# Optimization experiments

Hardware: AMD Instinct MI355X
Metric: run time of the kernel (lower is better)

## Reference

```python
import jax, jax.numpy as jnp
import numpy as np

SR = 24000
N_FFT = 1024
HOP = 320
N_MELS = 128
N_CB = 4
VOCAB = 1024
D_MODEL = 512


def _mel_fbanks():
    # torchaudio melscale_fbanks defaults: htk mel scale, norm=None, f_min=0, f_max=sr/2
    n_freqs = N_FFT // 2 + 1
    all_freqs = np.linspace(0.0, SR / 2.0, n_freqs)
    hz2mel = lambda f: 2595.0 * np.log10(1.0 + f / 700.0)
    m_pts = np.linspace(hz2mel(0.0), hz2mel(SR / 2.0), N_MELS + 2)
    f_pts = 700.0 * (10.0 ** (m_pts / 2595.0) - 1.0)
    f_diff = np.diff(f_pts)
    slopes = f_pts[None, :] - all_freqs[:, None]          # (n_freqs, n_mels+2)
    down = -slopes[:, :-2] / f_diff[:-1]
    up = slopes[:, 2:] / f_diff[1:]
    return np.maximum(0.0, np.minimum(down, up)).astype(np.float32)  # (n_freqs, n_mels)

_FB = jnp.asarray(_mel_fbanks())
# periodic Hann window (torch.hann_window default)
_WIN = jnp.asarray((0.5 * (1.0 - np.cos(2.0 * np.pi * np.arange(N_FFT) / N_FFT))).astype(np.float32))


def _log_mel(wav):
    # wav: (B, L). center=True STFT with reflect padding, power=2 spectrogram.
    pad = N_FFT // 2
    x = jnp.pad(wav, ((0, 0), (pad, pad)), mode='reflect')
    n_frames = 1 + (x.shape[1] - N_FFT) // HOP
    idx = HOP * jnp.arange(n_frames)[:, None] + jnp.arange(N_FFT)[None, :]
    frames = x[:, idx] * _WIN                              # (B, T, n_fft)
    spec = jnp.abs(jnp.fft.rfft(frames, axis=-1)) ** 2     # (B, T, n_freqs)
    mel = spec @ _FB                                       # (B, T, n_mels)
    return jnp.log(jnp.clip(mel, 1e-5))


def _conv1d(x, w, b):
    # x: (B, C, T), w: (O, I, 3), padding=1
    y = jax.lax.conv_general_dilated(x, w, window_strides=(1,), padding=((1, 1),),
                                     dimension_numbers=('NCH', 'OIH', 'NCH'))
    return y + b[None, :, None]


def setup_inputs() -> dict:
    key = jax.random.key(0)
    k = jax.random.split(key, 4)
    waveform = jax.random.normal(k[0], (16, 240000), dtype=jnp.float32)
    w1 = jax.random.normal(k[1], (256, N_MELS, 3), dtype=jnp.float32) * 0.05
    b1 = jnp.zeros((256,), dtype=jnp.float32)
    w2 = jax.random.normal(k[2], (D_MODEL, 256, 3), dtype=jnp.float32) * 0.05
    b2 = jnp.zeros((D_MODEL,), dtype=jnp.float32)
    codebooks = jax.random.normal(k[3], (N_CB, VOCAB, D_MODEL // N_CB), dtype=jnp.float32)
    return {"waveform": waveform, "w1": w1, "b1": b1, "w2": w2, "b2": b2, "codebooks": codebooks}


def reference(waveform, w1, b1, w2, b2, codebooks):
    logmel = _log_mel(waveform)                            # (B, T, n_mels)
    x = logmel.transpose(0, 2, 1)                          # (B, n_mels, T)
    h = jax.nn.gelu(_conv1d(x, w1, b1), approximate=False)
    feats = _conv1d(h, w2, b2).transpose(0, 2, 1)          # (B, T, D_MODEL)
    B, T, D = feats.shape
    f4 = feats.reshape(B, T, N_CB, D // N_CB)              # per-codebook slices
    x2 = jnp.sum(f4 * f4, axis=-1)[..., None]              # (B, T, K, 1)
    c2 = jnp.sum(codebooks * codebooks, axis=-1)           # (K, V)
    xc = jnp.einsum('btkd,kvd->btkv', f4, codebooks)       # (B, T, K, V)
    d2 = x2 - 2.0 * xc + c2[None, None]
    tokens = jnp.argmin(d2, axis=-1)                       # (B, T, K)
    return tokens.transpose(0, 2, 1).astype(jnp.int32)     # (B, n_codebooks, T)
```

## Files before the change

kernel.cpp:

```cpp
#include <hip/hip_runtime.h>
#include <hip/hip_bf16.h>
#include <float.h>

#define PI_D 3.14159265358979323846

#define LWAV 240000
#define TFR  751
#define BATCH 16
#define MROWS (BATCH * TFR)
#define NMEL 128
#define TFRP 753
#define PITCH2 12160
#define MTILES 95
#define MAXW 40

#define BSWZ(c) ((c) ^ ((((c) >> 5) & 3) << 2))

#define OFF_WIN    0u
#define OFF_TW512  4096u
#define OFF_UTW    8192u
#define OFF_C2MX   12304u
#define OFF_CNT    12352u
#define OFF_MELW   16384u
#define OFF_MELSL  36864u
#define OFF_WB1    40960u
#define OFF_WBH2   434176u
#define OFF_WBL2   1220608u
#define OFF_PB     434176u
#define OFF_C2     2007040u
#define OFF_CBH    2023424u
#define OFF_CBL    3072000u
#define OFF_X2     4120576u
#define OFF_HT     4317184u
#define OFF_FET    16777216u
#define OFF_LMT    OFF_FET
#define OFF_LIST   OFF_FET
#define WS_NEEDED  41685000u

typedef unsigned short u16;
typedef __attribute__((ext_vector_type(8))) __bf16 bf16x8;
typedef __attribute__((ext_vector_type(4))) float f32x4;
union UB { uint4 u; bf16x8 v; };
union UA { u16 s[8]; bf16x8 v; };

__device__ __forceinline__ u16 bf16rne(float x) {
  unsigned u = __float_as_uint(x);
  return (u16)((u + 0x7FFFu + ((u >> 16) & 1u)) >> 16);
}
__device__ __forceinline__ float bf16tof(u16 h) {
  return __uint_as_float(((unsigned)h) << 16);
}

__global__ void k_setup_tab(float* __restrict__ win, float2* __restrict__ tw512,
                            float2* __restrict__ utw) {
  int t = threadIdx.x;
  if (t < 1024) {
    double v = 0.5 * (1.0 - cos(2.0 * PI_D * (double)t / 1024.0));
    win[t] = (float)v;
  }
  if (t < 512) {
    double a = -2.0 * PI_D * (double)t / 512.0;
    tw512[t] = make_float2((float)cos(a), (float)sin(a));
  }
  if (t < 513) {
    double a = -2.0 * PI_D * (double)t / 1024.0;
    utw[t] = make_float2((float)cos(a), (float)sin(a));
  }
}

__device__ __forceinline__ double fpt_d(int j) {
  double melmax = 2595.0 * log10(1.0 + 12000.0 / 700.0);
  double mp = melmax * (double)j / 129.0;
  return 700.0 * (pow(10.0, mp / 2595.0) - 1.0);
}

__global__ void k_melw(float* __restrict__ melw, int2* __restrict__ melsl) {
  int m = threadIdx.x;
  double f0 = fpt_d(m), f1 = fpt_d(m + 1), f2 = fpt_d(m + 2);
  const double binw = 12000.0 / 512.0;
  int s = (int)floor(f0 / binw) + 1;
  if (s < 0) s = 0;
  int e = (int)ceil(f2 / binw) - 1;
  if (e > 512) e = 512;
  int len = e - s + 1;
  if (len < 0) len = 0;
  if (len > MAXW) len = MAXW;
  melsl[m] = make_int2(s, len);
  for (int j = 0; j < MAXW; ++j) {
    double freq = binw * (double)(s + j);
    double down = (freq - f0) / (f1 - f0);
    double up = (f2 - freq) / (f2 - f1);
    double v = fmin(down, up);
    v = fmax(0.0, v);
    melw[m * MAXW + j] = (j < len) ? (float)v : 0.f;
  }
}

__global__ void k_wt(const float* __restrict__ w, float* __restrict__ wt,
                     int O, int C) {
  int idx = blockIdx.x * 256 + threadIdx.x;
  int total = O * C * 3;
  if (idx >= total) return;
  int o = idx % O;
  int rest = idx / O;
  int i = rest % C;
  int dt = rest / C;
  wt[(dt * C + i) * O + o] = w[(o * C + i) * 3 + dt];
}

__global__ void k_wt2conv(const float* __restrict__ w2, u16* __restrict__ wbH2,
                          u16* __restrict__ wbL2) {
  int idx = blockIdx.x * 256 + threadIdx.x;
  if (idx >= 512 * 768) return;
  int o = idx / 768;
  int k = idx - o * 768;
  int dt = k >> 8, i = k & 255;
  float x = w2[(size_t)(o * 256 + i) * 3 + dt];
  u16 hh = bf16rne(x);
  wbH2[idx] = hh;
  wbL2[idx] = bf16rne(x - bf16tof(hh));
}

__global__ void k_c2(const float* __restrict__ cb, float* __restrict__ c2) {
  int v = blockIdx.x * 256 + threadIdx.x;
  if (v >= 4096) return;
  const float* r = cb + (size_t)v * 128;
  float s = 0.f;
#pragma unroll 8
  for (int i = 0; i < 128; ++i) s = fmaf(r[i], r[i], s);
  c2[v] = s;
}

__global__ void k_c2mx(const float* __restrict__ c2, float* __restrict__ c2mx,
                       unsigned* __restrict__ cnt) {
  __shared__ float red[256];
  int cb = blockIdx.x, tid = threadIdx.x;
  float m = 0.f;
  for (int v = tid; v < 1024; v += 256) m = fmaxf(m, c2[cb * 1024 + v]);
  red[tid] = m;
  __syncthreads();
  for (int s = 128; s > 0; s >>= 1) {
    if (tid < s) red[tid] = fmaxf(red[tid], red[tid + s]);
    __syncthreads();
  }
  if (tid == 0) {
    c2mx[cb] = red[0];
    if (cb == 0) *cnt = 0u;
  }
}

__global__ void k_cbconv(const float* __restrict__ cbs, u16* __restrict__ cbH,
                         u16* __restrict__ cbL) {
  int id = blockIdx.x * 256 + threadIdx.x;
  int v = id >> 5, d4 = (id & 31) * 4;
  float4 x = *(const float4*)(cbs + (size_t)v * 128 + d4);
  const float xs[4] = {x.x, x.y, x.z, x.w};
  unsigned wh[2], wl[2];
#pragma unroll
  for (int p = 0; p < 2; ++p) {
    u16 h0 = bf16rne(xs[2 * p]);
    u16 h1 = bf16rne(xs[2 * p + 1]);
    u16 l0 = bf16rne(xs[2 * p] - bf16tof(h0));
    u16 l1 = bf16rne(xs[2 * p + 1] - bf16tof(h1));
    wh[p] = (unsigned)h0 | ((unsigned)h1 << 16);
    wl[p] = (unsigned)l0 | ((unsigned)l1 << 16);
  }
  *(uint2*)(cbH + (size_t)v * 128 + d4) = make_uint2(wh[0], wh[1]);
  *(uint2*)(cbL + (size_t)v * 128 + d4) = make_uint2(wl[0], wl[1]);
}

__global__ void k_zerocols(float* __restrict__ a, int rows) {
  int tid = blockIdx.x * 256 + threadIdx.x;
  int col_id = tid & 31;
  int r = tid >> 5;
  if (r >= rows) return;
  int bq = col_id >> 1;
  int c = bq * TFRP + ((col_id & 1) ? 752 : 0);
  a[(size_t)r * PITCH2 + c] = 0.f;
}

__device__ __forceinline__ float2 cadd(float2 a, float2 b) { return make_float2(a.x + b.x, a.y + b.y); }
__device__ __forceinline__ float2 csub(float2 a, float2 b) { return make_float2(a.x - b.x, a.y - b.y); }
__device__ __forceinline__ float2 cmul(float2 a, float2 b) {
  return make_float2(a.x * b.x - a.y * b.y, a.x * b.y + a.y * b.x);
}
__device__ __forceinline__ float2 mulnegi(float2 a) { return make_float2(a.y, -a.x); }

__device__ __forceinline__ void dft8(const float2* d, float2* o) {
  const float S = 0.70710678118654752440f;
  float2 f0 = cadd(d[0], d[4]), f1 = csub(d[0], d[4]);
  float2 f2 = cadd(d[2], d[6]), f3 = csub(d[2], d[6]);
  float2 h0 = cadd(d[1], d[5]), h1 = csub(d[1], d[5]);
  float2 h2 = cadd(d[3], d[7]), h3 = csub(d[3], d[7]);
  float2 E0 = cadd(f0, f2), E2 = csub(f0, f2);
  float2 nif3 = mulnegi(f3);
  float2 E1 = cadd(f1, nif3), E3 = csub(f1, nif3);
  float2 O0 = cadd(h0, h2), O2 = csub(h0, h2);
  float2 nih3 = mulnegi(h3);
  float2 O1 = cadd(h1, nih3), O3 = csub(h1, nih3);
  float2 w1o = make_float2(S * (O1.x + O1.y), S * (O1.y - O1.x));
  float2 w2o = mulnegi(O2);
  float2 w3o = make_float2(S * (O3.y - O3.x), -S * (O3.x + O3.y));
  o[0] = cadd(E0, O0);  o[4] = csub(E0, O0);
  o[1] = cadd(E1, w1o); o[5] = csub(E1, w1o);
  o[2] = cadd(E2, w2o); o[6] = csub(E2, w2o);
  o[3] = cadd(E3, w3o); o[7] = csub(E3, w3o);
}

__device__ __forceinline__ float powspec(const float2* Z, const float2* __restrict__ utw,
                                         int k) {
  float2 Zk = Z[k & 511];
  float2 Zm = Z[(512 - k) & 511];
  float2 ut = utw[k];
  float fer = 0.5f * (Zk.x + Zm.x);
  float fei = 0.5f * (Zk.y - Zm.y);
  float fo_r = 0.5f * (Zk.y + Zm.y);
  float fo_i = -0.5f * (Zk.x - Zm.x);
  float xr = fer + ut.x * fo_r - ut.y * fo_i;
  float xi = fei + ut.x * fo_i + ut.y * fo_r;
  return xr * xr + xi * xi;
}

__global__ __launch_bounds__(256) void k_logmel3(
    const float* __restrict__ wav, const float* __restrict__ win,
    const float2* __restrict__ tw512, const float2* __restrict__ utw,
    const float* __restrict__ melw, const int2* __restrict__ melsl,
    float* __restrict__ lmT) {
  __shared__ float2 zbuf[4][512];
  __shared__ float pbuf[4][516];
  __shared__ float mex[128][5];

  const int w = threadIdx.x >> 6;
  const int t = threadIdx.x & 63;
  const int bq = blockIdx.x / 188;
  const int t0 = (blockIdx.x % 188) * 4;
  const int tt = min(t0 + w, TFR - 1);
  const float* wv = wav + (size_t)bq * LWAV;
  float2* Z = zbuf[w];
  float* p = pbuf[w];

  const int base = tt * 320 - 512;

  float2 c[8];
  if (base >= 0 && base + 1024 <= LWAV) {
    const float2* wv2 = (const float2*)(wv + base);
    const float2* wn2 = (const float2*)win;
#pragma unroll
    for (int j = 0; j < 8; ++j) {
      int mm = t + 64 * j;
      float2 xv = wv2[mm];
      float2 wn = wn2[mm];
      c[j] = make_float2(xv.x * wn.x, xv.y * wn.y);
    }
  } else {
#pragma unroll
    for (int j = 0; j < 8; ++j) {
      int mm = t + 64 * j;
      int n0 = base + 2 * mm, n1 = n0 + 1;
      int j0 = n0 < 0 ? -n0 : (n0 >= LWAV ? 2 * LWAV - 2 - n0 : n0);
      int j1 = n1 < 0 ? -n1 : (n1 >= LWAV ? 2 * LWAV - 2 - n1 : n1);
      c[j] = make_float2(wv[j0] * win[2 * mm], wv[j1] * win[2 * mm + 1]);
    }
  }

  float2 e[8];
  dft8(c, e);
#pragma unroll
  for (int pp = 1; pp < 8; ++pp) e[pp] = cmul(e[pp], tw512[(t * pp) & 511]);
#pragma unroll
  for (int pp = 0; pp < 8; ++pp) Z[pp * 64 + (t ^ (pp << 3))] = e[pp];
  asm volatile("s_waitcnt lgkmcnt(0)" ::: "memory");

  const int P = t >> 3, M = t & 7;
  float2 g[8];
#pragma unroll
  for (int v = 0; v < 8; ++v) g[v] = Z[P * 64 + ((M + 8 * v) ^ (P << 3))];
  asm volatile("s_waitcnt lgkmcnt(0)" ::: "memory");

  float2 y[8];
  dft8(g, y);
#pragma unroll
  for (int aa = 1; aa < 8; ++aa) y[aa] = cmul(y[aa], tw512[(8 * M * aa) & 511]);
#pragma unroll
  for (int aa = 0; aa < 8; ++aa) Z[aa * 64 + (((M << 3) + P) ^ (aa << 3))] = y[aa];
  asm volatile("s_waitcnt lgkmcnt(0)" ::: "memory");

  float2 yv[8];
#pragma unroll
  for (int u = 0; u < 8; ++u) yv[u] = Z[P * 64 + (((u << 3) + M) ^ (P << 3))];
  asm volatile("s_waitcnt lgkmcnt(0)" ::: "memory");

  float2 X[8];
  dft8(yv, X);
#pragma unroll
  for (int bb = 0; bb < 8; ++bb) Z[bb * 64 + t] = X[bb];
  asm volatile("s_waitcnt lgkmcnt(0)" ::: "memory");

#pragma unroll
  for (int j = 0; j < 8; ++j) {
    int k = t + 64 * j;
    p[k] = powspec(Z, utw, k);
  }
  if (t == 0) p[512] = powspec(Z, utw, 512);
  asm volatile("s_waitcnt lgkmcnt(0)" ::: "memory");

#pragma unroll
  for (int h = 0; h < 2; ++h) {
    int m = 2 * t + h;
    int2 sl = melsl[m];
    float acc = 0.f;
    const float* wrow = melw + m * MAXW;
    for (int j = 0; j < sl.y; ++j) acc = fmaf(p[sl.x + j], wrow[j], acc);
    mex[m][w] = logf(fmaxf(acc, 1e-5f));
  }
  __syncthreads();
  if (threadIdx.x < 128) {
    int cc = threadIdx.x;
    float* op = lmT + (size_t)cc * PITCH2 + (size_t)bq * TFRP + 1 + t0;
    op[0] = mex[cc][0];
    op[1] = mex[cc][1];
    op[2] = mex[cc][2];
    op[3] = mex[cc][3];
  }
}

template <int C, int N, int BN, bool GELU>
__global__ __launch_bounds__(256) void k_conv64(const float* __restrict__ in,
                                                const float* __restrict__ wt,
                                                const float* __restrict__ bias,
                                                float* __restrict__ out) {
  constexpr int K = 3 * C;
  constexpr int NC = BN / 16;
  __shared__ float At[32 * 64];
  __shared__ float Bt[32 * BN];
  const int m0 = blockIdx.x * 64;
  const int n0 = blockIdx.y * BN;
  const int tid = threadIdx.x;
  const int tm = tid >> 4, tn = tid & 15;

  int bco[NC / 4];
#pragma unroll
  for (int i = 0; i < NC / 4; ++i) bco[i] = BSWZ(tn * NC + i * 4);

  float acc[4][NC] = {};

  for (int k0 = 0; k0 < K; k0 += 32) {
    const int dt = k0 / C;
    const int i0 = k0 - dt * C;
    const float* asrc = in + (size_t)i0 * PITCH2 + (m0 + dt - 1);
    const float* bsrc = wt + (size_t)k0 * N + n0;
#pragma unroll
    for (int h = 0; h < 2; ++h) {
      const int id = tid + h * 256;
      const int r = id >> 4, cf = (id & 15) * 4;
      const float* ap = asrc + (size_t)r * PITCH2 + cf;
      *(float4*)&At[r * 64 + cf] = make_float4(ap[0], ap[1], ap[2], ap[3]);
    }
#pragma unroll
    for (int h = 0; h < BN / 32; ++h) {
      const int id = tid + h * 256;
      const int r = id / (BN / 4), cf = (id % (BN / 4)) * 4;
      *(float4*)&Bt[r * BN + BSWZ(cf)] = *(const float4*)(bsrc + (size_t)r * N + cf);
    }
    __syncthreads();
#pragma unroll
    for (int kc = 0; kc < 32; ++kc) {
      float4 a = *(const float4*)&At[kc * 64 + tm * 4];
      float av[4] = {a.x, a.y, a.z, a.w};
      float bv[NC];
#pragma unroll
      for (int i = 0; i < NC / 4; ++i) {
        float4 b = *(const float4*)&Bt[kc * BN + bco[i]];
        bv[i * 4] = b.x; bv[i * 4 + 1] = b.y; bv[i * 4 + 2] = b.z; bv[i * 4 + 3] = b.w;
      }
#pragma unroll
      for (int r = 0; r < 4; ++r)
#pragma unroll
        for (int cq = 0; cq < NC; ++cq) acc[r][cq] = fmaf(av[r], bv[cq], acc[r][cq]);
    }
    __syncthreads();
  }

#pragma unroll
  for (int cq = 0; cq < NC; ++cq) {
    const int n = n0 + tn * NC + cq;
    const float bb = bias[n];
    float vv[4];
#pragma unroll
    for (int r = 0; r < 4; ++r) {
      float v = acc[r][cq] + bb;
      if (GELU) v = 0.5f * v * (1.0f + erff(v * 0.7071067811865476f));
      vv[r] = v;
    }
    *(float4*)(out + (size_t)n * PITCH2 + m0 + tm * 4) =
        make_float4(vv[0], vv[1], vv[2], vv[3]);
  }
}

#define MFMA16(a, b, c) __builtin_amdgcn_mfma_f32_16x16x32_bf16((a), (b), (c), 0, 0, 0)

#define C2M_ISSUE_A(dst, cc) do {                                           \
    const int kc0_ = (cc) * 32;                                             \
    const int dt_ = kc0_ >> 8, i0_ = kc0_ & 255;                            \
    const float* hb_ = hT + (size_t)(i0_ + g * 8) * PITCH2                  \
                       + m0 + mhalf * 32 + ln + dt_ - 1;                    \
    _Pragma("unroll") for (int mi_ = 0; mi_ < 2; ++mi_)                     \
      _Pragma("unroll") for (int j_ = 0; j_ < 8; ++j_)                      \
        dst[mi_][j_] = hb_[(size_t)j_ * PITCH2 + mi_ * 16];                 \
  } while (0)

#define C2M_ISSUE_B(cc) do {                                                \
    const int kc0_ = (cc) * 32;                                             \
    _Pragma("unroll") for (int h2_ = 0; h2_ < 2; ++h2_) {                   \
      const int id_ = tid + h2_ * 256;                                      \
      const int nn_ = id_ >> 2, part_ = id_ & 3;                            \
      const size_t src_ = (size_t)(n0 + nn_) * 768 + kc0_ + part_ * 8;      \
      rBh[h2_] = *(const uint4*)(wbH2 + src_);                              \
      rBl[h2_] = *(const uint4*)(wbL2 + src_);                              \
    }                                                                       \
  } while (0)

#define C2M_COMMIT_B(buf) do {                                              \
    _Pragma("unroll") for (int h2_ = 0; h2_ < 2; ++h2_) {                   \
      const int id_ = tid + h2_ * 256;                                      \
      const int nn_ = id_ >> 2, part_ = id_ & 3;                            \
      *(uint4*)&bHs[buf][nn_ * 40 + part_ * 8] = rBh[h2_];                  \
      *(uint4*)&bLs[buf][nn_ * 40 + part_ * 8] = rBl[h2_];                  \
    }                                                                       \
  } while (0)

__global__ __launch_bounds__(256) void k_conv2m(
    const float* __restrict__ hT,
    const u16* __restrict__ wbH2, const u16* __restrict__ wbL2,
    const float* __restrict__ b2, float* __restrict__ feT) {
  __shared__ __align__(16) u16 bHs[2][128 * 40];
  __shared__ __align__(16) u16 bLs[2][128 * 40];
  const int nq = blockIdx.x;
  const int mt = blockIdx.y;
  const int tid = threadIdx.x;
  const int w = tid >> 6, l = tid & 63;
  const int mhalf = w & 1, nhalf = w >> 1;
  const int g = l >> 4, ln = l & 15;
  const int m0 = mt * 64;
  const int n0 = nq * 128;

  f32x4 acc[2][4];
#pragma unroll
  for (int mi = 0; mi < 2; ++mi)
#pragma unroll
    for (int vi = 0; vi < 4; ++vi) acc[mi][vi] = (f32x4){0.f, 0.f, 0.f, 0.f};

  float rA[2][8], rA2[2][8];
  uint4 rBh[2], rBl[2];

  C2M_ISSUE_A(rA, 0);
  C2M_ISSUE_B(0);
  C2M_COMMIT_B(0);
  __syncthreads();

  int cur = 0;
  for (int cc = 0; cc < 24; ++cc) {
    const bool more = (cc + 1 < 24);
    if (more) { C2M_ISSUE_B(cc + 1); C2M_ISSUE_A(rA2, cc + 1); }
    UA aH[2], aL[2];
#pragma unroll
    for (int mi = 0; mi < 2; ++mi)
#pragma unroll
      for (int j = 0; j < 8; ++j) {
        u16 hh = bf16rne(rA[mi][j]);
        aH[mi].s[j] = hh;
        aL[mi].s[j] = bf16rne(rA[mi][j] - bf16tof(hh));
      }
    const u16* bH = bHs[cur];
    const u16* bL = bLs[cur];
#pragma unroll
    for (int vi = 0; vi < 4; ++vi) {
      const int nn = nhalf * 64 + vi * 16 + ln;
      UB bh, bl;
      bh.u = *(const uint4*)&bH[nn * 40 + g * 8];
      bl.u = *(const uint4*)&bL[nn * 40 + g * 8];
#pragma unroll
      for (int mi = 0; mi < 2; ++mi) {
        acc[mi][vi] = MFMA16(aH[mi].v, bh.v, acc[mi][vi]);
        acc[mi][vi] = MFMA16(aH[mi].v, bl.v, acc[mi][vi]);
        acc[mi][vi] = MFMA16(aL[mi].v, bh.v, acc[mi][vi]);
      }
    }
    if (more) {
      C2M_COMMIT_B(cur ^ 1);
      __syncthreads();
      cur ^= 1;
#pragma unroll
      for (int mi = 0; mi < 2; ++mi)
#pragma unroll
        for (int j = 0; j < 8; ++j) rA[mi][j] = rA2[mi][j];
    }
  }

#pragma unroll
  for (int vi = 0; vi < 4; ++vi) {
    const int nn = n0 + nhalf * 64 + vi * 16 + ln;
    const float bb = b2[nn];
#pragma unroll
    for (int mi = 0; mi < 2; ++mi) {
      f32x4 A = acc[mi][vi];
      *(float4*)(feT + (size_t)nn * PITCH2 + m0 + mhalf * 32 + mi * 16 + g * 4) =
          make_float4(A[0] + bb, A[1] + bb, A[2] + bb, A[3] + bb);
    }
  }
}

__global__ void k_x2(const float* __restrict__ feT, float* __restrict__ x2) {
  int m = blockIdx.x * 256 + threadIdx.x;
  int cb = blockIdx.y;
  if (m >= PITCH2) return;
  const float* p = feT + (size_t)(cb * 128) * PITCH2 + m;
  float s = 0.f;
#pragma unroll 4
  for (int r = 0; r < 128; ++r) {
    float a = p[(size_t)r * PITCH2];
    s = fmaf(a, a, s);
  }
  x2[(size_t)cb * PITCH2 + m] = s;
}

__global__ __launch_bounds__(256) void k_vqmfma(
    const float* __restrict__ feT,
    const u16* __restrict__ cbH, const u16* __restrict__ cbL,
    const float* __restrict__ c2, float4* __restrict__ pb) {
  __shared__ __align__(16) u16 bHs[64 * 128];
  __shared__ __align__(16) u16 bLs[64 * 128];
  __shared__ float trip[64][2][4];

  const int vh = blockIdx.x;
  const int mt = blockIdx.y;
  const int cb = blockIdx.z;
  const int tid = threadIdx.x;
  const int w = tid >> 6, l = tid & 63;
  const int mhalf = w & 1, vhalf = w >> 1;
  const int m0 = mt * 64;
  const int q0 = vh * 8, q1 = q0 + 8;

  UA aH[2][4], aL[2][4];
  {
    const int g = l >> 4;
    const float* fb = feT + (size_t)(cb * 128 + (g << 3)) * PITCH2
                      + m0 + mhalf * 32 + (l & 15);
#pragma unroll
    for (int mi = 0; mi < 2; ++mi) {
#pragma unroll
      for (int ks = 0; ks < 4; ++ks) {
#pragma unroll
        for (int j = 0; j < 8; ++j) {
          float x = fb[(size_t)(ks * 32 + j) * PITCH2 + mi * 16];
          u16 hh = bf16rne(x);
          aH[mi][ks].s[j] = hh;
          aL[mi][ks].s[j] = bf16rne(x - bf16tof(hh));
        }
      }
    }
  }

  {
    const u16* gh = cbH + (size_t)(cb * 1024 + q0 * 64) * 128;
    const u16* gl = cbL + (size_t)(cb * 1024 + q0 * 64) * 128;
#pragma unroll
    for (int h = 0; h < 4; ++h) {
      int id = tid + h * 256;
      int row = id >> 4, c16 = id & 15;
      int go = row * 128 + c16 * 8;
      int so = row * 128 + ((c16 * 8) ^ ((row & 7) << 3));
      *(uint4*)&bHs[so] = *(const uint4*)&gh[go];
      *(uint4*)&bLs[so] = *(const uint4*)&gl[go];
    }
  }
  __syncthreads();

  float sb1[8], sb2[8];
  int si1[8];
#pragma unroll
  for (int st = 0; st < 8; ++st) { sb1[st] = FLT_MAX; sb2[st] = FLT_MAX; si1[st] = 0; }

  f32x4 acc[2][2];
#pragma unroll
  for (int mi = 0; mi < 2; ++mi)
#pragma unroll
    for (int vi = 0; vi < 2; ++vi) acc[mi][vi] = (f32x4){0.f, 0.f, 0.f, 0.f};

  const float* c2b = c2 + cb * 1024;

  for (int q = q0; q < q1; ++q) {
#pragma unroll
    for (int ks = 0; ks < 4; ++ks) {
      const int kbx = (ks * 32 + ((l >> 4) << 3)) ^ ((l & 7) << 3);
      const int rb = vhalf * 32 + (l & 15);
      UB b0h, b0l, b1h, b1l;
      b0h.u = *(const uint4*)&bHs[rb * 128 + kbx];
      b0l.u = *(const uint4*)&bLs[rb * 128 + kbx];
      b1h.u = *(const uint4*)&bHs[(rb + 16) * 128 + kbx];
      b1l.u = *(const uint4*)&bLs[(rb + 16) * 128 + kbx];
      acc[0][0] = MFMA16(aH[0][ks].v, b0h.v, acc[0][0]);
      acc[0][0] = MFMA16(aH[0][ks].v, b0l.v, acc[0][0]);
      acc[0][0] = MFMA16(aL[0][ks].v, b0h.v, acc[0][0]);
      acc[0][1] = MFMA16(aH[0][ks].v, b1h.v, acc[0][1]);
      acc[0][1] = MFMA16(aH[0][ks].v, b1l.v, acc[0][1]);
      acc[0][1] = MFMA16(aL[0][ks].v, b1h.v, acc[0][1]);
      acc[1][0] = MFMA16(aH[1][ks].v, b0h.v, acc[1][0]);
      acc[1][0] = MFMA16(aH[1][ks].v, b0l.v, acc[1][0]);
      acc[1][0] = MFMA16(aL[1][ks].v, b0h.v, acc[1][0]);
      acc[1][1] = MFMA16(aH[1][ks].v, b1h.v, acc[1][1]);
      acc[1][1] = MFMA16(aH[1][ks].v, b1l.v, acc[1][1]);
      acc[1][1] = MFMA16(aL[1][ks].v, b1h.v, acc[1][1]);
    }

#pragma unroll
    for (int mi = 0; mi < 2; ++mi) {
#pragma unroll
      for (int vi = 0; vi < 2; ++vi) {
        const int vg = q * 64 + vhalf * 32 + vi * 16 + (l & 15);
        const float cv = c2b[vg];
        f32x4 A = acc[mi][vi];
#pragma unroll
        for (int j = 0; j < 4; ++j) {
          const float s = fmaf(-2.f, A[j], cv);
          const int st = mi * 4 + j;
          if (s < sb1[st]) { sb2[st] = sb1[st]; sb1[st] = s; si1[st] = vg; }
          else { sb2[st] = fminf(sb2[st], s); }
        }
        acc[mi][vi] = (f32x4){0.f, 0.f, 0.f, 0.f};
      }
    }

    if (q + 1 < q1) {
      __syncthreads();
      const u16* gh = cbH + (size_t)(cb * 1024 + (q + 1) * 64) * 128;
      const u16* gl = cbL + (size_t)(cb * 1024 + (q + 1) * 64) * 128;
#pragma unroll
      for (int h = 0; h < 4; ++h) {
        int id = tid + h * 256;
        int row = id >> 4, c16 = id & 15;
        int go = row * 128 + c16 * 8;
        int so = row * 128 + ((c16 * 8) ^ ((row & 7) << 3));
        *(uint4*)&bHs[so] = *(const uint4*)&gh[go];
        *(uint4*)&bLs[so] = *(const uint4*)&gl[go];
      }
      __syncthreads();
    }
  }

#pragma unroll
  for (int st = 0; st < 8; ++st) {
    float B1 = sb1[st], B2 = sb2[st];
    int I1 = si1[st];
#pragma unroll
    for (int off = 1; off < 16; off <<= 1) {
      float oB1 = __shfl_xor(B1, off, 64);
      int oI1 = __shfl_xor(I1, off, 64);
      float oB2 = __shfl_xor(B2, off, 64);
      bool take = (oB1 < B1) || (oB1 == B1 && oI1 < I1);
      float lose = take ? B1 : oB1;
      B2 = fminf(fminf(B2, oB2), lose);
      if (take) { B1 = oB1; I1 = oI1; }
    }
    if ((l & 15) == 0) {
      int row = mhalf * 32 + (st >> 2) * 16 + (l >> 4) * 4 + (st & 3);
      trip[row][vhalf][0] = B1;
      trip[row][vhalf][1] = __int_as_float(I1);
      trip[row][vhalf][2] = B2;
    }
  }
  __syncthreads();
  if (tid < 64) {
    float B1 = trip[tid][0][0], B2 = trip[tid][0][2];
    int I1 = __float_as_int(trip[tid][0][1]);
    float oB1 = trip[tid][1][0], oB2 = trip[tid][1][2];
    int oI1 = __float_as_int(trip[tid][1][1]);
    bool take = (oB1 < B1) || (oB1 == B1 && oI1 < I1);
    float lose = take ? B1 : oB1;
    B2 = fminf(fminf(B2, oB2), lose);
    if (take) { B1 = oB1; I1 = oI1; }
    pb[(size_t)(cb * 2 + vh) * PITCH2 + m0 + tid] =
        make_float4(B1, __int_as_float(I1), B2, 0.f);
  }
}

#define LISTCAP 48064u
__global__ void k_vqsel(const float4* __restrict__ pb, const float* __restrict__ x2,
                        const float* __restrict__ c2mx, unsigned* __restrict__ cnt,
                        unsigned* __restrict__ list, int* __restrict__ out) {
  int ml = blockIdx.x * 256 + threadIdx.x;
  int cb = blockIdx.y;
  if (ml >= MROWS) return;
  int b = ml / TFR, t = ml - b * TFR;
  int mp = b * TFRP + 1 + t;

  float B1 = FLT_MAX, B2 = FLT_MAX;
  int I1 = 0;
#pragma unroll
  for (int vh = 0; vh < 2; ++vh) {
    float4 e = pb[(size_t)(cb * 2 + vh) * PITCH2 + mp];
    float a1 = e.x, a2 = e.z;
    int ai = __float_as_int(e.y);
    if (a1 < B1 || (a1 == B1 && ai < I1)) {
      B2 = fminf(B1, a2);
      B1 = a1;
      I1 = ai;
    } else {
      B2 = fminf(B2, a1);
    }
  }

  float xx = x2[(size_t)cb * PITCH2 + mp];
  float cm = c2mx[cb];
  float eps = 1.5e-4f * sqrtf(fmaxf(xx * cm, 0.f)) + 6e-5f * (xx + cm);
  if (!(B2 - B1 > eps)) {
    unsigned k = atomicAdd(cnt, 1u);
    if (k < LISTCAP) list[k] = ((unsigned)cb << 14) | (unsigned)mp;
  }
  out[((size_t)b * 4 + cb) * TFR + t] = I1;
}

__global__ __launch_bounds__(256) void k_vqfix(
    const unsigned* __restrict__ cnt, const unsigned* __restrict__ list,
    const float* __restrict__ hT, const float* __restrict__ w2,
    const float* __restrict__ b2, const float* __restrict__ cbs,
    const float* __restrict__ c2, int* __restrict__ out) {
  __shared__ float xs[128];
  __shared__ float rd[256];
  __shared__ int ri[256];
  const int tid = threadIdx.x;
  const unsigned n = min(*cnt, LISTCAP);
  for (unsigned i = blockIdx.x; i < n; i += gridDim.x) {
    unsigned e = list[i];
    int cb = e >> 14;
    int mp = e & 0x3FFF;
    __syncthreads();
    if (tid < 128) {
      int o = cb * 128 + tid;
      float dot = 0.f;
      for (int dt = 0; dt < 3; ++dt) {
        const float* hp = hT + (mp + dt - 1);
        const float* wp = w2 + (size_t)o * 256 * 3 + dt;
#pragma unroll 8
        for (int ii = 0; ii < 256; ++ii)
          dot = fmaf(hp[(size_t)ii * PITCH2], wp[(size_t)ii * 3], dot);
      }
      xs[tid] = dot + b2[o];
    }
    __syncthreads();
    float xx = 0.f;
#pragma unroll 8
    for (int d = 0; d < 128; ++d) xx = fmaf(xs[d], xs[d], xx);
    float bd = FLT_MAX;
    int bi = 0;
#pragma unroll
    for (int vv = 0; vv < 4; ++vv) {
      int v = tid * 4 + vv;
      const float* cp = cbs + (size_t)(cb * 1024 + v) * 128;
      float dot = 0.f;
#pragma unroll 8
      for (int d = 0; d < 128; ++d) dot = fmaf(xs[d], cp[d], dot);
      float d2 = xx - 2.f * dot + c2[cb * 1024 + v];
      if (d2 < bd) { bd = d2; bi = v; }
    }
    rd[tid] = bd;
    ri[tid] = bi;
    __syncthreads();
    for (int s = 128; s > 0; s >>= 1) {
      if (tid < s) {
        float od = rd[tid + s];
        int oi = ri[tid + s];
        if (od < rd[tid] || (od == rd[tid] && oi < ri[tid])) { rd[tid] = od; ri[tid] = oi; }
      }
      __syncthreads();
    }
    if (tid == 0) {
      int b = mp / TFRP, t = mp % TFRP - 1;
      out[((size_t)b * 4 + cb) * TFR + t] = ri[0];
    }
  }
}

extern "C" void kernel_launch(void* const* d_in, const int* in_sizes, int n_in,
                              void* d_out, int out_size, void* d_ws, size_t ws_size,
                              hipStream_t stream) {
  if (ws_size < WS_NEEDED) return;

  const float* wav = (const float*)d_in[0];
  const float* w1 = (const float*)d_in[1];
  const float* b1 = (const float*)d_in[2];
  const float* w2 = (const float*)d_in[3];
  const float* b2 = (const float*)d_in[4];
  const float* cbs = (const float*)d_in[5];
  int* out = (int*)d_out;

  char* W = (char*)d_ws;
  float* win = (float*)(W + OFF_WIN);
  float2* tw512 = (float2*)(W + OFF_TW512);
  float2* utw = (float2*)(W + OFF_UTW);
  float* c2mx = (float*)(W + OFF_C2MX);
  unsigned* cnt = (unsigned*)(W + OFF_CNT);
  float* melw = (float*)(W + OFF_MELW);
  int2* melsl = (int2*)(W + OFF_MELSL);
  float* wb1 = (float*)(W + OFF_WB1);
  u16* wbH2 = (u16*)(W + OFF_WBH2);
  u16* wbL2 = (u16*)(W + OFF_WBL2);
  float4* pb = (float4*)(W + OFF_PB);
  unsigned* list = (unsigned*)(W + OFF_LIST);
  float* c2 = (float*)(W + OFF_C2);
  u16* cbH = (u16*)(W + OFF_CBH);
  u16* cbL = (u16*)(W + OFF_CBL);
  float* x2 = (float*)(W + OFF_X2);
  float* hT = (float*)(W + OFF_HT);
  float* feT = (float*)(W + OFF_FET);
  float* lmT = (float*)(W + OFF_LMT);

  k_setup_tab<<<1, 1024, 0, stream>>>(win, tw512, utw);
  k_melw<<<1, 128, 0, stream>>>(melw, melsl);
  k_wt<<<(256 * 128 * 3 + 255) / 256, 256, 0, stream>>>(w1, wb1, 256, 128);
  k_wt2conv<<<1536, 256, 0, stream>>>(w2, wbH2, wbL2);
  k_c2<<<16, 256, 0, stream>>>(cbs, c2);
  k_c2mx<<<4, 256, 0, stream>>>(c2, c2mx, cnt);
  k_cbconv<<<512, 256, 0, stream>>>(cbs, cbH, cbL);

  k_logmel3<<<16 * 188, 256, 0, stream>>>(wav, win, tw512, utw, melw, melsl, lmT);
  k_zerocols<<<(128 * 32 + 255) / 256, 256, 0, stream>>>(lmT, 128);
  k_conv64<128, 256, 64, true><<<dim3(190, 4), 256, 0, stream>>>(lmT, wb1, b1, hT);
  k_zerocols<<<(256 * 32 + 255) / 256, 256, 0, stream>>>(hT, 256);
  k_conv2m<<<dim3(4, 190), 256, 0, stream>>>(hT, wbH2, wbL2, b2, feT);

  k_x2<<<dim3((PITCH2 + 255) / 256, 4), 256, 0, stream>>>(feT, x2);
  k_vqmfma<<<dim3(2, 190, 4), 256, 0, stream>>>(feT, cbH, cbL, c2, pb);
  k_vqsel<<<dim3((MROWS + 255) / 256, 4), 256, 0, stream>>>(pb, x2, c2mx, cnt, list, out);
  k_vqfix<<<1024, 256, 0, stream>>>(cnt, list, hT, w2, b2, cbs, c2, out);
}
```

Before: 297.3 us.

## Transpose conv2 weights and codebooks for coalesced access in VQ fix-up kernel

The fallback VQ fix-up kernel now reads transposed fp32 copies of the conv2 weights and codebooks, so adjacent threads touch adjacent addresses. It also stages the input column of hT in shared memory, and the grid grows from 1024 to 2048 blocks. The aim is to remove strided, uncoalesced global loads in the recompute path. In exchange, two extra transpose kernels run every call, adding about 3.5 MB of writes and the matching reads, which could cost more than the fix-up saves when the list is short.

```diff
diff --git a/kernel.cpp b/kernel.cpp
--- a/kernel.cpp
+++ b/kernel.cpp
@@ -35,6 +35,8 @@
 #define OFF_FET    16777216u
 #define OFF_LMT    OFF_FET
 #define OFF_LIST   OFF_FET
+#define OFF_WT2F   (OFF_FET + 262144u)
+#define OFF_CBTF   18612224u
 #define WS_NEEDED  41685000u
 
 typedef unsigned short u16;
@@ -119,6 +121,22 @@
   u16 hh = bf16rne(x);
   wbH2[idx] = hh;
   wbL2[idx] = bf16rne(x - bf16tof(hh));
+}
+
+__global__ void k_wt2f(const float* __restrict__ w2, float* __restrict__ wt2f) {
+  int idx = blockIdx.x * 256 + threadIdx.x;
+  if (idx >= 768 * 512) return;
+  int o = idx & 511, k = idx >> 9;
+  int dt = k >> 8, i = k & 255;
+  wt2f[idx] = w2[(size_t)(o * 256 + i) * 3 + dt];
+}
+
+__global__ void k_cbtf(const float* __restrict__ cbs, float* __restrict__ cbTf) {
+  int idx = blockIdx.x * 256 + threadIdx.x;
+  int v = idx & 1023;
+  int d = (idx >> 10) & 127;
+  int cb = idx >> 17;
+  cbTf[idx] = cbs[(size_t)((cb << 10) + v) * 128 + d];
 }
 
 __global__ void k_c2(const float* __restrict__ cb, float* __restrict__ c2) {
@@ -722,9 +740,10 @@
 
 __global__ __launch_bounds__(256) void k_vqfix(
     const unsigned* __restrict__ cnt, const unsigned* __restrict__ list,
-    const float* __restrict__ hT, const float* __restrict__ w2,
-    const float* __restrict__ b2, const float* __restrict__ cbs,
+    const float* __restrict__ hT, const float* __restrict__ wt2f,
+    const float* __restrict__ b2, const float* __restrict__ cbTf,
     const float* __restrict__ c2, int* __restrict__ out) {
+  __shared__ float hcol[768];
   __shared__ float xs[128];
   __shared__ float rd[256];
   __shared__ int ri[256];
@@ -735,32 +754,38 @@
     int cb = e >> 14;
     int mp = e & 0x3FFF;
     __syncthreads();
+#pragma unroll
+    for (int h = 0; h < 3; ++h) {
+      int kk = tid + h * 256;
+      int dt = kk >> 8, ii = kk & 255;
+      hcol[kk] = hT[(size_t)ii * PITCH2 + (mp + dt - 1)];
+    }
+    __syncthreads();
     if (tid < 128) {
       int o = cb * 128 + tid;
       float dot = 0.f;
-      for (int dt = 0; dt < 3; ++dt) {
-        const float* hp = hT + (mp + dt - 1);
-        const float* wp = w2 + (size_t)o * 256 * 3 + dt;
-#pragma unroll 8
-        for (int ii = 0; ii < 256; ++ii)
-          dot = fmaf(hp[(size_t)ii * PITCH2], wp[(size_t)ii * 3], dot);
-      }
+      for (int k = 0; k < 768; ++k)
+        dot = fmaf(hcol[k], wt2f[(size_t)k * 512 + o], dot);
       xs[tid] = dot + b2[o];
     }
     __syncthreads();
     float xx = 0.f;
 #pragma unroll 8
     for (int d = 0; d < 128; ++d) xx = fmaf(xs[d], xs[d], xx);
+    float dot4[4] = {0.f, 0.f, 0.f, 0.f};
+    const float* cbase = cbTf + (size_t)(cb * 128) * 1024 + tid;
+    for (int d = 0; d < 128; ++d) {
+      const float* cp = cbase + (size_t)d * 1024;
+      float x = xs[d];
+#pragma unroll
+      for (int vv = 0; vv < 4; ++vv) dot4[vv] = fmaf(x, cp[vv * 256], dot4[vv]);
+    }
     float bd = FLT_MAX;
     int bi = 0;
 #pragma unroll
     for (int vv = 0; vv < 4; ++vv) {
-      int v = tid * 4 + vv;
-      const float* cp = cbs + (size_t)(cb * 1024 + v) * 128;
-      float dot = 0.f;
-#pragma unroll 8
-      for (int d = 0; d < 128; ++d) dot = fmaf(xs[d], cp[d], dot);
-      float d2 = xx - 2.f * dot + c2[cb * 1024 + v];
+      int v = vv * 256 + tid;
+      float d2 = xx - 2.f * dot4[vv] + c2[cb * 1024 + v];
       if (d2 < bd) { bd = d2; bi = v; }
     }
     rd[tid] = bd;
@@ -807,6 +832,8 @@
   u16* wbL2 = (u16*)(W + OFF_WBL2);
   float4* pb = (float4*)(W + OFF_PB);
   unsigned* list = (unsigned*)(W + OFF_LIST);
+  float* wt2f = (float*)(W + OFF_WT2F);
+  float* cbTf = (float*)(W + OFF_CBTF);
   float* c2 = (float*)(W + OFF_C2);
   u16* cbH = (u16*)(W + OFF_CBH);
   u16* cbL = (u16*)(W + OFF_CBL);
@@ -831,6 +858,8 @@
 
   k_x2<<<dim3((PITCH2 + 255) / 256, 4), 256, 0, stream>>>(feT, x2);
   k_vqmfma<<<dim3(2, 190, 4), 256, 0, stream>>>(feT, cbH, cbL, c2, pb);
+  k_wt2f<<<1536, 256, 0, stream>>>(w2, wt2f);
+  k_cbtf<<<2048, 256, 0, stream>>>(cbs, cbTf);
   k_vqsel<<<dim3((MROWS + 255) / 256, 4), 256, 0, stream>>>(pb, x2, c2mx, cnt, list, out);
-  k_vqfix<<<1024, 256, 0, stream>>>(cnt, list, hT, w2, b2, cbs, c2, out);
-}
+  k_vqfix<<<2048, 256, 0, stream>>>(cnt, list, hT, wt2f, b2, cbTf, c2, out);
+}
```

Measured after the change: 273.5 us. 1.09x faster.
